# Kernel tuning notes

Hardware: AMD Instinct MI355X
Metric: run time of the kernel (lower is better)

Reference implementation:

```python
import math
import jax, jax.numpy as jnp
import numpy as np

B = 8          # number of graphs in the batch
NMAX = 256     # max nodes per graph (padding size)
K = 128        # num_kernels
H = 32         # num_heads
NTYPE = 101    # max_node_type + 1


def setup_inputs() -> dict:
    key = jax.random.key(0)
    ks = jax.random.split(key, 10)
    sizes = np.asarray(NMAX - np.arange(B) * 16, dtype=np.int32)  # 256,240,...,144 -> ragged
    N = int(sizes.sum())  # 1600
    coord = jax.random.normal(ks[0], (N, 3), dtype=jnp.float32) * 3.0
    node_type = jax.random.randint(ks[1], (N,), 0, NTYPE, dtype=jnp.int32)
    gaussian_means = jax.random.uniform(ks[2], (1, K), minval=0.0, maxval=3.0, dtype=jnp.float32)
    gaussian_stds = jax.random.uniform(ks[3], (1, K), minval=0.0, maxval=3.0, dtype=jnp.float32)
    # nn.Embedding(max_node_type+1, 2) tables; original init is const(0)/const(1),
    # we perturb so the computation is non-degenerate.
    mul_w = jax.random.normal(ks[4], (NTYPE, 2), dtype=jnp.float32) * 0.1
    bias_w = 1.0 + jax.random.normal(ks[5], (NTYPE, 2), dtype=jnp.float32) * 0.1
    W1 = jax.random.normal(ks[6], (K, K), dtype=jnp.float32) / math.sqrt(K)
    b1 = jnp.zeros((K,), dtype=jnp.float32)
    W2 = jax.random.normal(ks[7], (K, H), dtype=jnp.float32) / math.sqrt(K)
    b2 = jnp.zeros((H,), dtype=jnp.float32)
    return {
        "coord": coord,
        "gaussian_means": gaussian_means,
        "gaussian_stds": gaussian_stds,
        "mul_w": mul_w,
        "bias_w": bias_w,
        "W1": W1,
        "b1": b1,
        "W2": W2,
        "b2": b2,
        "node_type": node_type,
        "batch_num_nodes": jnp.asarray(sizes),
    }


def reference(coord, gaussian_means, gaussian_stds, mul_w, bias_w, W1, b1, W2, b2,
              node_type, batch_num_nodes):
    N = coord.shape[0]
    offsets = jnp.concatenate([jnp.zeros((1,), dtype=batch_num_nodes.dtype),
                               jnp.cumsum(batch_num_nodes)[:-1]])
    ar = jnp.arange(NMAX)
    idx = offsets[:, None] + ar[None, :]                     # [B, n] flat node index per graph slot
    valid = ar[None, :] < batch_num_nodes[:, None]           # [B, n] node mask
    idx_c = jnp.clip(idx, 0, N - 1)
    pc = coord[idx_c]                                        # [B, n, 3] padded coords
    pt = node_type[idx_c]                                    # [B, n]

    # pairwise Euclidean distance (torch.cdist p=2), sqrt-safe at 0
    diff = pc[:, :, None, :] - pc[:, None, :, :]             # [B, n, n, 3]
    sq = jnp.sum(diff * diff, axis=-1)                       # [B, n, n]
    nz = sq > 0
    dist = jnp.where(nz, jnp.sqrt(jnp.where(nz, sq, 1.0)), 0.0)

    # outer-sum of per-node (src, dst) scaling embeddings
    mul_e = mul_w[pt]                                        # [B, n, 2]
    bias_e = bias_w[pt]
    mul = mul_e[:, :, None, 0] + mul_e[:, None, :, 1]        # [B, n, n]
    bias = bias_e[:, :, None, 0] + bias_e[:, None, :, 1]
    scaled = mul * dist + bias                               # [B, n, n]

    means = gaussian_means.reshape(-1)                       # [K]
    stds = jnp.abs(gaussian_stds.reshape(-1)) + 0.01         # [K]
    z = (scaled[..., None] - means) / stds                   # [B, n, n, K]
    gk = jnp.exp(-0.5 * z * z) / (-math.sqrt(2.0 * math.pi) * stds)

    h = jax.nn.gelu(gk @ W1 + b1, approximate=False)         # exact gelu like torch F.gelu
    out = h @ W2 + b2                                        # [B, n, n, H]

    pair = valid[:, :, None] & valid[:, None, :]             # padded positions -> -inf
    return jnp.where(pair[..., None], out, -jnp.inf)
```

## Files before the change

kernel.cpp:

```cpp
#include <hip/hip_runtime.h>
#include <math.h>

#define NMAXC 256
#define KC 128
#define HC 32
#define BC 8
#define TP 128
#define NEG_SENTINEL (-1.0e30f)
#define LOG2E 1.4426950408889634f

typedef __bf16 bf16x8 __attribute__((ext_vector_type(8)));
typedef float  f32x16 __attribute__((ext_vector_type(16)));
union FragU { uint4 u; bf16x8 v; };

#if __has_builtin(__builtin_amdgcn_exp2f)
#define EXP2F(x) __builtin_amdgcn_exp2f(x)
#else
#define EXP2F(x) exp2f(x)
#endif

__device__ __forceinline__ unsigned pack2(float lo, float hi) {
    return __builtin_amdgcn_perm(__float_as_uint(hi), __float_as_uint(lo), 0x07060302u);
}

__device__ __forceinline__ int swap23(int k) {
    return (k & ~12) | ((k & 4) << 1) | ((k & 8) >> 1);
}

__global__ __launch_bounds__(256) void se3d_prep(const float* __restrict__ W1,
                                                 const float* __restrict__ W2,
                                                 const float* __restrict__ gm,
                                                 const float* __restrict__ gs,
                                                 unsigned* __restrict__ wsu) {
    int t = blockIdx.x * 256 + threadIdx.x;
    if (t < 2048) {
        int fb = t >> 6, lane = t & 63;
        int nt = fb >> 3, ks = fb & 7;
        int n  = nt * 32 + (lane & 31);
        int k0 = ks * 16 + 8 * (lane >> 5);
        unsigned u[4];
#pragma unroll
        for (int p = 0; p < 4; ++p)
            u[p] = pack2(-W1[(k0 + 2 * p) * KC + n], -W1[(k0 + 2 * p + 1) * KC + n]);
        ((uint4*)wsu)[t] = make_uint4(u[0], u[1], u[2], u[3]);
    } else if (t < 2560) {
        int c = t - 2048;
        int ks = c >> 6, lane = c & 63;
        int n  = lane & 31;
        int k0 = ks * 16 + 8 * (lane >> 5);
        unsigned u[4];
#pragma unroll
        for (int p = 0; p < 4; ++p) {
            int ta = swap23(k0 + 2 * p);
            int tb = swap23(k0 + 2 * p + 1);
            u[p] = pack2(W2[ta * HC + n], W2[tb * HC + n]);
        }
        ((uint4*)wsu)[2048 + c] = make_uint4(u[0], u[1], u[2], u[3]);
    } else if (t < 2688) {
        int k = t - 2560;
        float inv = 1.0f / (fabsf(gs[k]) + 0.01f);
        float m  = gm[k];
        float A2 = -0.5f * inv * inv * LOG2E;
        float* wf = (float*)wsu + 10240;
        wf[2 * k]     = A2;
        wf[2 * k + 1] = -2.0f * A2 * m;
        wf[256 + k]   = A2 * m * m + log2f(0.3989422804014327f * inv);
    }
}

__global__ __launch_bounds__(256, 4) void se3d_main(
    const float* __restrict__ coord, const float* __restrict__ mulw,
    const float* __restrict__ biasw, const float* __restrict__ b1,
    const float* __restrict__ b2, const int* __restrict__ ntype,
    const int* __restrict__ bnn, const void* __restrict__ ws,
    float* __restrict__ out)
{
    __shared__ float scaled[TP];
    __shared__ int   obase[TP];
    __shared__ float cAB[2 * KC];
    __shared__ float cC[KC];

    const int b = blockIdx.y;
    const int n = bnn[b];
    const int q0 = blockIdx.x * TP;
    const int tid = threadIdx.x;

    if (q0 >= n * n) {
        int v = q0 + (tid >> 1) - n * n;
        int wdt = 256 - n;
        int na = n * wdt;
        int i, j;
        if (v < na) { i = v / wdt; j = n + (v - i * wdt); }
        else        { int vp = v - na; i = n + (vp >> 8); j = vp & 255; }
        float4 s4 = make_float4(NEG_SENTINEL, NEG_SENTINEL, NEG_SENTINEL, NEG_SENTINEL);
        float4* o = (float4*)(out + ((size_t)((b * NMAXC + i) * NMAXC + j)) * HC)
                  + (tid & 1) * 4;
#pragma unroll
        for (int t = 0; t < 4; ++t) o[t] = s4;
        return;
    }

    int off = 0;
    for (int t = 0; t < b; ++t) off += bnn[t];

    const float* wf = (const float*)((const char*)ws + 40960);
    if (tid < 2 * KC) cAB[tid] = wf[tid];
    if (tid < KC) {
        cC[tid] = wf[256 + tid];
        int q = q0 + tid;
        int i = q / n;
        int j = q - i * n;
        int gi = off + i, gj = off + j;
        float dx = coord[gi * 3 + 0] - coord[gj * 3 + 0];
        float dy = coord[gi * 3 + 1] - coord[gj * 3 + 1];
        float dz = coord[gi * 3 + 2] - coord[gj * 3 + 2];
        float sq = dx * dx + dy * dy + dz * dz;
        float dist = sq > 0.f ? sqrtf(sq) : 0.f;
        int ti = ntype[gi], tj = ntype[gj];
        scaled[tid] = (mulw[ti * 2 + 0] + mulw[tj * 2 + 1]) * dist
                    + (biasw[ti * 2 + 0] + biasw[tj * 2 + 1]);
        obase[tid]  = ((b * NMAXC + i) * NMAXC + j) * HC;
    }
    __syncthreads();

    const int l = tid & 63, w = tid >> 6;
    const int hi = l >> 5, ln31 = l & 31;
    const int m0 = w * 32;
    const float s = scaled[m0 + ln31];

    const bf16x8* wsW1 = (const bf16x8*)ws;
    const bf16x8* wsW2 = (const bf16x8*)((const char*)ws + 32768);

    FragU gfr[8];
#pragma unroll
    for (int ks = 0; ks < 8; ++ks) {
        int k0 = ks * 16 + 8 * hi;
        const float4* ab = (const float4*)(cAB + 2 * k0);
        const float4* cc = (const float4*)(cC + k0);
        float4 ab0 = ab[0], ab1 = ab[1], ab2 = ab[2], ab3 = ab[3];
        float4 c0 = cc[0], c1 = cc[1];
        float t0 = EXP2F(fmaf(fmaf(ab0.x, s, ab0.y), s, c0.x));
        float t1 = EXP2F(fmaf(fmaf(ab0.z, s, ab0.w), s, c0.y));
        float t2 = EXP2F(fmaf(fmaf(ab1.x, s, ab1.y), s, c0.z));
        float t3 = EXP2F(fmaf(fmaf(ab1.z, s, ab1.w), s, c0.w));
        float t4 = EXP2F(fmaf(fmaf(ab2.x, s, ab2.y), s, c1.x));
        float t5 = EXP2F(fmaf(fmaf(ab2.z, s, ab2.w), s, c1.y));
        float t6 = EXP2F(fmaf(fmaf(ab3.x, s, ab3.y), s, c1.z));
        float t7 = EXP2F(fmaf(fmaf(ab3.z, s, ab3.w), s, c1.w));
        gfr[ks].u.x = pack2(t0, t1);
        gfr[ks].u.y = pack2(t2, t3);
        gfr[ks].u.z = pack2(t4, t5);
        gfr[ks].u.w = pack2(t6, t7);
    }

    const float KSG = -1.702f * LOG2E;
    f32x16 c2;
#pragma unroll
    for (int g = 0; g < 4; ++g) {
        float4 t4 = *(const float4*)(b2 + 8 * g + 4 * hi);
        c2[4 * g + 0] = t4.x; c2[4 * g + 1] = t4.y;
        c2[4 * g + 2] = t4.z; c2[4 * g + 3] = t4.w;
    }

#define GELU_PACK(AA, F0, F1) do {                                      \
    float vv[16];                                                       \
    _Pragma("unroll")                                                   \
    for (int r = 0; r < 16; ++r) {                                      \
        float x = AA[r];                                                \
        float e = EXP2F(x * KSG);                                       \
        vv[r] = x * __builtin_amdgcn_rcpf(1.0f + e);                    \
    }                                                                   \
    F0.u.x = pack2(vv[0],  vv[1]);  F0.u.y = pack2(vv[2],  vv[3]);      \
    F0.u.z = pack2(vv[4],  vv[5]);  F0.u.w = pack2(vv[6],  vv[7]);      \
    F1.u.x = pack2(vv[8],  vv[9]);  F1.u.y = pack2(vv[10], vv[11]);     \
    F1.u.z = pack2(vv[12], vv[13]); F1.u.w = pack2(vv[14], vv[15]);     \
} while (0)

#pragma unroll
    for (int tp = 0; tp < 2; ++tp) {
        f32x16 a0, a1;
#pragma unroll
        for (int g = 0; g < 4; ++g) {
            float4 t0 = *(const float4*)(b1 + (2 * tp)     * 32 + 8 * g + 4 * hi);
            float4 t1 = *(const float4*)(b1 + (2 * tp + 1) * 32 + 8 * g + 4 * hi);
            a0[4 * g + 0] = t0.x; a0[4 * g + 1] = t0.y;
            a0[4 * g + 2] = t0.z; a0[4 * g + 3] = t0.w;
            a1[4 * g + 0] = t1.x; a1[4 * g + 1] = t1.y;
            a1[4 * g + 2] = t1.z; a1[4 * g + 3] = t1.w;
        }
#pragma unroll
        for (int ks = 0; ks < 8; ++ks) {
            bf16x8 w0 = wsW1[((2 * tp)     * 8 + ks) * 64 + l];
            bf16x8 w1 = wsW1[((2 * tp + 1) * 8 + ks) * 64 + l];
            a0 = __builtin_amdgcn_mfma_f32_32x32x16_bf16(w0, gfr[ks].v, a0, 0, 0, 0);
            a1 = __builtin_amdgcn_mfma_f32_32x32x16_bf16(w1, gfr[ks].v, a1, 0, 0, 0);
        }
        FragU f00, f01, f10, f11;
        GELU_PACK(a0, f00, f01);
        GELU_PACK(a1, f10, f11);
        c2 = __builtin_amdgcn_mfma_f32_32x32x16_bf16(wsW2[(4 * tp + 0) * 64 + l], f00.v, c2, 0, 0, 0);
        c2 = __builtin_amdgcn_mfma_f32_32x32x16_bf16(wsW2[(4 * tp + 1) * 64 + l], f01.v, c2, 0, 0, 0);
        c2 = __builtin_amdgcn_mfma_f32_32x32x16_bf16(wsW2[(4 * tp + 2) * 64 + l], f10.v, c2, 0, 0, 0);
        c2 = __builtin_amdgcn_mfma_f32_32x32x16_bf16(wsW2[(4 * tp + 3) * 64 + l], f11.v, c2, 0, 0, 0);
    }
#undef GELU_PACK

    const int ob = obase[m0 + ln31];
    float* op = out + (size_t)ob + 4 * hi;
#pragma unroll
    for (int g = 0; g < 4; ++g) {
        *(float4*)(op + 8 * g) =
            make_float4(c2[4 * g], c2[4 * g + 1], c2[4 * g + 2], c2[4 * g + 3]);
    }
}

extern "C" void kernel_launch(void* const* d_in, const int* in_sizes, int n_in,
                              void* d_out, int out_size, void* d_ws, size_t ws_size,
                              hipStream_t stream) {
    const float* coord = (const float*)d_in[0];
    const float* gm    = (const float*)d_in[1];
    const float* gs    = (const float*)d_in[2];
    const float* mulw  = (const float*)d_in[3];
    const float* biasw = (const float*)d_in[4];
    const float* W1    = (const float*)d_in[5];
    const float* b1    = (const float*)d_in[6];
    const float* W2    = (const float*)d_in[7];
    const float* b2    = (const float*)d_in[8];
    const int* ntype   = (const int*)d_in[9];
    const int* bnn     = (const int*)d_in[10];
    float* out = (float*)d_out;

    hipLaunchKernelGGL(se3d_prep, dim3(11), dim3(256), 0, stream,
                       W1, W2, gm, gs, (unsigned*)d_ws);
    hipLaunchKernelGGL(se3d_main, dim3(NMAXC * NMAXC / TP, BC), dim3(256),
                       0, stream,
                       coord, mulw, biasw, b1, b2, ntype, bnn, d_ws, out);
}
```

Before: 122.6 us.

## Process two 32-pair tiles per wave to reuse W1/W2 fragments across MFMAs

Each block now handles 256 pairs instead of 128, so each wave computes two 32-row tiles (A and B). Each W1 and W2 fragment loaded from global memory feeds two MFMAs, halving weight-fragment loads per pair. The padding-fill path now has each thread write a full 128-byte row. Register pressure roughly doubles for gaussian fragments and accumulators, so launch bounds drop from 4 to 3 blocks per CU, and the grid presumably needs adjusting in the host code.

```diff
diff --git a/kernel.cpp b/kernel.cpp
--- a/kernel.cpp
+++ b/kernel.cpp
@@ -5,7 +5,7 @@
 #define KC 128
 #define HC 32
 #define BC 8
-#define TP 128
+#define TP 256
 #define NEG_SENTINEL (-1.0e30f)
 #define LOG2E 1.4426950408889634f
 
@@ -68,7 +68,7 @@
     }
 }
 
-__global__ __launch_bounds__(256, 4) void se3d_main(
+__global__ __launch_bounds__(256, 3) void se3d_main(
     const float* __restrict__ coord, const float* __restrict__ mulw,
     const float* __restrict__ biasw, const float* __restrict__ b1,
     const float* __restrict__ b2, const int* __restrict__ ntype,
@@ -86,17 +86,16 @@
     const int tid = threadIdx.x;
 
     if (q0 >= n * n) {
-        int v = q0 + (tid >> 1) - n * n;
+        int v = q0 + tid - n * n;
         int wdt = 256 - n;
         int na = n * wdt;
         int i, j;
         if (v < na) { i = v / wdt; j = n + (v - i * wdt); }
         else        { int vp = v - na; i = n + (vp >> 8); j = vp & 255; }
         float4 s4 = make_float4(NEG_SENTINEL, NEG_SENTINEL, NEG_SENTINEL, NEG_SENTINEL);
-        float4* o = (float4*)(out + ((size_t)((b * NMAXC + i) * NMAXC + j)) * HC)
-                  + (tid & 1) * 4;
-#pragma unroll
-        for (int t = 0; t < 4; ++t) o[t] = s4;
+        float4* o = (float4*)(out + ((size_t)((b * NMAXC + i) * NMAXC + j)) * HC);
+#pragma unroll
+        for (int t = 0; t < 8; ++t) o[t] = s4;
         return;
     }
 
@@ -104,9 +103,9 @@
     for (int t = 0; t < b; ++t) off += bnn[t];
 
     const float* wf = (const float*)((const char*)ws + 40960);
-    if (tid < 2 * KC) cAB[tid] = wf[tid];
-    if (tid < KC) {
-        cC[tid] = wf[256 + tid];
+    cAB[tid] = wf[tid];
+    if (tid < KC) cC[tid] = wf[256 + tid];
+    {
         int q = q0 + tid;
         int i = q / n;
         int j = q - i * n;
@@ -125,13 +124,14 @@
 
     const int l = tid & 63, w = tid >> 6;
     const int hi = l >> 5, ln31 = l & 31;
-    const int m0 = w * 32;
-    const float s = scaled[m0 + ln31];
+    const int m0 = w * 64;
+    const float sA = scaled[m0 + ln31];
+    const float sB = scaled[m0 + 32 + ln31];
 
     const bf16x8* wsW1 = (const bf16x8*)ws;
     const bf16x8* wsW2 = (const bf16x8*)((const char*)ws + 32768);
 
-    FragU gfr[8];
+    FragU gfrA[8], gfrB[8];
 #pragma unroll
     for (int ks = 0; ks < 8; ++ks) {
         int k0 = ks * 16 + 8 * hi;
@@ -139,27 +139,34 @@
         const float4* cc = (const float4*)(cC + k0);
         float4 ab0 = ab[0], ab1 = ab[1], ab2 = ab[2], ab3 = ab[3];
         float4 c0 = cc[0], c1 = cc[1];
-        float t0 = EXP2F(fmaf(fmaf(ab0.x, s, ab0.y), s, c0.x));
-        float t1 = EXP2F(fmaf(fmaf(ab0.z, s, ab0.w), s, c0.y));
-        float t2 = EXP2F(fmaf(fmaf(ab1.x, s, ab1.y), s, c0.z));
-        float t3 = EXP2F(fmaf(fmaf(ab1.z, s, ab1.w), s, c0.w));
-        float t4 = EXP2F(fmaf(fmaf(ab2.x, s, ab2.y), s, c1.x));
-        float t5 = EXP2F(fmaf(fmaf(ab2.z, s, ab2.w), s, c1.y));
-        float t6 = EXP2F(fmaf(fmaf(ab3.x, s, ab3.y), s, c1.z));
-        float t7 = EXP2F(fmaf(fmaf(ab3.z, s, ab3.w), s, c1.w));
-        gfr[ks].u.x = pack2(t0, t1);
-        gfr[ks].u.y = pack2(t2, t3);
-        gfr[ks].u.z = pack2(t4, t5);
-        gfr[ks].u.w = pack2(t6, t7);
+#pragma unroll
+        for (int grp = 0; grp < 2; ++grp) {
+            float s = grp ? sB : sA;
+            float t0 = EXP2F(fmaf(fmaf(ab0.x, s, ab0.y), s, c0.x));
+            float t1 = EXP2F(fmaf(fmaf(ab0.z, s, ab0.w), s, c0.y));
+            float t2 = EXP2F(fmaf(fmaf(ab1.x, s, ab1.y), s, c0.z));
+            float t3 = EXP2F(fmaf(fmaf(ab1.z, s, ab1.w), s, c0.w));
+            float t4 = EXP2F(fmaf(fmaf(ab2.x, s, ab2.y), s, c1.x));
+            float t5 = EXP2F(fmaf(fmaf(ab2.z, s, ab2.w), s, c1.y));
+            float t6 = EXP2F(fmaf(fmaf(ab3.x, s, ab3.y), s, c1.z));
+            float t7 = EXP2F(fmaf(fmaf(ab3.z, s, ab3.w), s, c1.w));
+            FragU& g = grp ? gfrB[ks] : gfrA[ks];
+            g.u.x = pack2(t0, t1);
+            g.u.y = pack2(t2, t3);
+            g.u.z = pack2(t4, t5);
+            g.u.w = pack2(t6, t7);
+        }
     }
 
     const float KSG = -1.702f * LOG2E;
-    f32x16 c2;
+    f32x16 c2A, c2B;
 #pragma unroll
     for (int g = 0; g < 4; ++g) {
         float4 t4 = *(const float4*)(b2 + 8 * g + 4 * hi);
-        c2[4 * g + 0] = t4.x; c2[4 * g + 1] = t4.y;
-        c2[4 * g + 2] = t4.z; c2[4 * g + 3] = t4.w;
+        c2A[4 * g + 0] = t4.x; c2A[4 * g + 1] = t4.y;
+        c2A[4 * g + 2] = t4.z; c2A[4 * g + 3] = t4.w;
+        c2B[4 * g + 0] = t4.x; c2B[4 * g + 1] = t4.y;
+        c2B[4 * g + 2] = t4.z; c2B[4 * g + 3] = t4.w;
     }
 
 #define GELU_PACK(AA, F0, F1) do {                                      \
@@ -177,40 +184,47 @@
 } while (0)
 
 #pragma unroll
-    for (int tp = 0; tp < 2; ++tp) {
-        f32x16 a0, a1;
+    for (int nt = 0; nt < 4; ++nt) {
+        f32x16 aA, aB;
 #pragma unroll
         for (int g = 0; g < 4; ++g) {
-            float4 t0 = *(const float4*)(b1 + (2 * tp)     * 32 + 8 * g + 4 * hi);
-            float4 t1 = *(const float4*)(b1 + (2 * tp + 1) * 32 + 8 * g + 4 * hi);
-            a0[4 * g + 0] = t0.x; a0[4 * g + 1] = t0.y;
-            a0[4 * g + 2] = t0.z; a0[4 * g + 3] = t0.w;
-            a1[4 * g + 0] = t1.x; a1[4 * g + 1] = t1.y;
-            a1[4 * g + 2] = t1.z; a1[4 * g + 3] = t1.w;
+            float4 t4 = *(const float4*)(b1 + nt * 32 + 8 * g + 4 * hi);
+            aA[4 * g + 0] = t4.x; aA[4 * g + 1] = t4.y;
+            aA[4 * g + 2] = t4.z; aA[4 * g + 3] = t4.w;
+            aB[4 * g + 0] = t4.x; aB[4 * g + 1] = t4.y;
+            aB[4 * g + 2] = t4.z; aB[4 * g + 3] = t4.w;
         }
 #pragma unroll
         for (int ks = 0; ks < 8; ++ks) {
-            bf16x8 w0 = wsW1[((2 * tp)     * 8 + ks) * 64 + l];
-            bf16x8 w1 = wsW1[((2 * tp + 1) * 8 + ks) * 64 + l];
-            a0 = __builtin_amdgcn_mfma_f32_32x32x16_bf16(w0, gfr[ks].v, a0, 0, 0, 0);
-            a1 = __builtin_amdgcn_mfma_f32_32x32x16_bf16(w1, gfr[ks].v, a1, 0, 0, 0);
-        }
-        FragU f00, f01, f10, f11;
-        GELU_PACK(a0, f00, f01);
-        GELU_PACK(a1, f10, f11);
-        c2 = __builtin_amdgcn_mfma_f32_32x32x16_bf16(wsW2[(4 * tp + 0) * 64 + l], f00.v, c2, 0, 0, 0);
-        c2 = __builtin_amdgcn_mfma_f32_32x32x16_bf16(wsW2[(4 * tp + 1) * 64 + l], f01.v, c2, 0, 0, 0);
-        c2 = __builtin_amdgcn_mfma_f32_32x32x16_bf16(wsW2[(4 * tp + 2) * 64 + l], f10.v, c2, 0, 0, 0);
-        c2 = __builtin_amdgcn_mfma_f32_32x32x16_bf16(wsW2[(4 * tp + 3) * 64 + l], f11.v, c2, 0, 0, 0);
+            bf16x8 w0 = wsW1[(nt * 8 + ks) * 64 + l];
+            aA = __builtin_amdgcn_mfma_f32_32x32x16_bf16(w0, gfrA[ks].v, aA, 0, 0, 0);
+            aB = __builtin_amdgcn_mfma_f32_32x32x16_bf16(w0, gfrB[ks].v, aB, 0, 0, 0);
+        }
+        FragU fA0, fA1, fB0, fB1;
+        GELU_PACK(aA, fA0, fA1);
+        GELU_PACK(aB, fB0, fB1);
+        bf16x8 u0 = wsW2[(2 * nt + 0) * 64 + l];
+        bf16x8 u1 = wsW2[(2 * nt + 1) * 64 + l];
+        c2A = __builtin_amdgcn_mfma_f32_32x32x16_bf16(u0, fA0.v, c2A, 0, 0, 0);
+        c2A = __builtin_amdgcn_mfma_f32_32x32x16_bf16(u1, fA1.v, c2A, 0, 0, 0);
+        c2B = __builtin_amdgcn_mfma_f32_32x32x16_bf16(u0, fB0.v, c2B, 0, 0, 0);
+        c2B = __builtin_amdgcn_mfma_f32_32x32x16_bf16(u1, fB1.v, c2B, 0, 0, 0);
     }
 #undef GELU_PACK
 
-    const int ob = obase[m0 + ln31];
-    float* op = out + (size_t)ob + 4 * hi;
-#pragma unroll
-    for (int g = 0; g < 4; ++g) {
-        *(float4*)(op + 8 * g) =
-            make_float4(c2[4 * g], c2[4 * g + 1], c2[4 * g + 2], c2[4 * g + 3]);
+    {
+        const int obA = obase[m0 + ln31];
+        float* opA = out + (size_t)obA + 4 * hi;
+#pragma unroll
+        for (int g = 0; g < 4; ++g)
+            *(float4*)(opA + 8 * g) =
+                make_float4(c2A[4 * g], c2A[4 * g + 1], c2A[4 * g + 2], c2A[4 * g + 3]);
+        const int obB = obase[m0 + 32 + ln31];
+        float* opB = out + (size_t)obB + 4 * hi;
+#pragma unroll
+        for (int g = 0; g < 4; ++g)
+            *(float4*)(opB + 8 * g) =
+                make_float4(c2B[4 * g], c2B[4 * g + 1], c2B[4 * g + 2], c2B[4 * g + 3]);
     }
 }
 
```

Result: no change. 121.7 us (-0.8%).
